# Kernel tuning notes

Measured on AMD Instinct MI355X. Metric: run time of the kernel, lower is better.

## Reference

```python
import jax, jax.numpy as jnp
import numpy as np

B, Lq, Lkv = 4, 1024, 4096
Cq, Ckv, E, NH = 512, 512, 512, 8
HD = E // NH


def setup_inputs() -> dict:
    key = jax.random.key(0)
    ks = jax.random.split(key, 8)
    s = 0.02
    return {
        "Xq": jax.random.normal(ks[0], (B, Lq, Cq), dtype=jnp.float32),
        "Xkv": jax.random.normal(ks[1], (B, Lkv, Ckv), dtype=jnp.float32),
        "mask": jax.random.randint(ks[2], (B, Lq, 1), 0, 2, dtype=jnp.int32),
        "Wq": jax.random.normal(ks[3], (Cq, E), dtype=jnp.float32) * s,
        "bq": jnp.zeros((E,), dtype=jnp.float32),
        "Wkv": jax.random.normal(ks[4], (Ckv, 2 * E), dtype=jnp.float32) * s,
        "bkv": jnp.zeros((2 * E,), dtype=jnp.float32),
        "Wp": jax.random.normal(ks[5], (E, E), dtype=jnp.float32) * s,
        "bp": jnp.zeros((E,), dtype=jnp.float32),
        "attn_pos": jax.random.normal(ks[6], (1, NH, Lq, Lkv), dtype=jnp.float32) * s,
    }


def reference(Xq, Xkv, mask, Wq, bq, Wkv, bkv, Wp, bp, attn_pos):
    scale = HD ** -0.5
    # projections
    Q = (Xq @ Wq + bq).reshape(B, Lq, NH, HD).transpose(0, 2, 1, 3) * scale  # [B,NH,Lq,HD]
    KV = (Xkv @ Wkv + bkv).reshape(B, Lkv, 2, NH, HD)
    K = KV[:, :, 0].transpose(0, 2, 1, 3)  # [B,NH,Lkv,HD]
    V = KV[:, :, 1].transpose(0, 2, 1, 3)
    # scores + learned positional bias
    attn = jnp.einsum('bhqd,bhkd->bhqk', Q, K) + attn_pos  # [B,NH,Lq,Lkv]
    # dummy-column masked softmax (mask: [B,Lq,1], 1=keep row)
    m = mask.astype(attn.dtype)[:, None]           # [B,1,Lq,1]
    attn = attn + (1.0 - m) * (-100.0)             # suppress masked query rows
    dummy = jnp.broadcast_to(jnp.where(m == 0, 100.0, -100.0), (B, NH, Lq, 1))
    attn = jax.nn.softmax(jnp.concatenate([attn, dummy], axis=-1), axis=-1)[..., :Lkv]
    # weighted sum + output projection (dropout = identity in eval)
    out = jnp.einsum('bhqk,bhkd->bhqd', attn, V)
    out = out.transpose(0, 2, 1, 3).reshape(B, Lq, E)
    return out @ Wp + bp
```

## Files before the change

### kernel.cpp

```cpp
#include <hip/hip_runtime.h>

typedef unsigned short u16;
typedef __attribute__((ext_vector_type(8))) short bf16x8;
typedef __attribute__((ext_vector_type(4))) float f32x4;
typedef __attribute__((ext_vector_type(2))) unsigned u32x2;
typedef __attribute__((ext_vector_type(4))) unsigned u32x4;

__device__ __forceinline__ u16 f2bf(float x) {
    union { float f; unsigned u; } v; v.f = x;
    unsigned r = v.u + 0x7FFF + ((v.u >> 16) & 1);
    return (u16)(r >> 16);
}

__device__ __forceinline__ unsigned cvt_pk_bf16(float lo, float hi) {
    unsigned r;
    asm("v_cvt_pk_bf16_f32 %0, %1, %2" : "=v"(r) : "v"(lo), "v"(hi));
    return r;
}

__device__ __forceinline__ bf16x8 pk8(const f32x4& s0, const f32x4& s1) {
    union { u32x4 u; bf16x8 v; } x;
    x.u[0] = cvt_pk_bf16(s0[0], s0[1]);
    x.u[1] = cvt_pk_bf16(s0[2], s0[3]);
    x.u[2] = cvt_pk_bf16(s1[0], s1[1]);
    x.u[3] = cvt_pk_bf16(s1[2], s1[3]);
    return x.v;
}

__device__ __forceinline__ void gl_lds16(const u16* g, u16* l) {
    __builtin_amdgcn_global_load_lds((const __attribute__((address_space(1))) void*)g,
                                     (__attribute__((address_space(3))) void*)l, 16, 0, 0);
}

__global__ __launch_bounds__(256) void prep_kernel(const float* __restrict__ Xq,
                                                   const float* __restrict__ Xkv,
                                                   u16* __restrict__ oq,
                                                   u16* __restrict__ okv,
                                                   const float* __restrict__ Wq,
                                                   const float* __restrict__ Wkv,
                                                   const float* __restrict__ Wp,
                                                   u16* __restrict__ WqT,
                                                   u16* __restrict__ WkvT,
                                                   u16* __restrict__ WpT) {
    __shared__ float tile[64][65];
    int bid = blockIdx.x;
    int tid = threadIdx.x;
    if (bid < 5120) {
        const float* in;
        u16* out;
        size_t i;
        if (bid < 1024) {
            in = Xq; out = oq;
            i = ((size_t)bid * 256 + tid) * 8;
        } else {
            in = Xkv; out = okv;
            i = ((size_t)(bid - 1024) * 256 + tid) * 8;
        }
        const float4* p = (const float4*)(in + i);
        float4 a = p[0], b = p[1];
        u32x4 w = {cvt_pk_bf16(a.x, a.y), cvt_pk_bf16(a.z, a.w),
                   cvt_pk_bf16(b.x, b.y), cvt_pk_bf16(b.z, b.w)};
        *(u32x4*)(out + i) = w;
        return;
    }
    bid -= 5120;
    const float* in;
    u16* out;
    int R = 512, C, bx, by;
    if (bid < 64) {
        in = Wq; out = WqT; C = 512; bx = bid & 7; by = bid >> 3;
    } else if (bid < 192) {
        bid -= 64;
        in = Wkv; out = WkvT; C = 1024; bx = bid & 15; by = bid >> 4;
    } else {
        bid -= 192;
        in = Wp; out = WpT; C = 512; bx = bid & 7; by = bid >> 3;
    }
    int r0 = by * 64, c0 = bx * 64;
#pragma unroll
    for (int j = 0; j < 16; ++j) {
        int e = tid + j * 256;
        int row = e >> 6, col = e & 63;
        tile[row][col] = in[(size_t)(r0 + row) * C + c0 + col];
    }
    __syncthreads();
#pragma unroll
    for (int j = 0; j < 16; ++j) {
        int e = tid + j * 256;
        int row = e >> 6, col = e & 63;
        out[(size_t)(c0 + row) * R + r0 + col] = f2bf(tile[col][row]);
    }
}

__global__ __launch_bounds__(256) void gemm_qkv(const u16* __restrict__ Xqb,
                                                const u16* __restrict__ WqT,
                                                const float* __restrict__ bq,
                                                u16* __restrict__ Qb,
                                                const u16* __restrict__ Xkvb,
                                                const u16* __restrict__ WkvT,
                                                const float* __restrict__ bkv,
                                                u16* __restrict__ Kb,
                                                u16* __restrict__ Vt) {
    __shared__ u16 Al[128][64];
    __shared__ u16 Bl[128][64];
    int tid = threadIdx.x;
    int lane = tid & 63, wid = tid >> 6;
    int wr = wid >> 1, wc = wid & 1;
    int l15 = lane & 15, g = lane >> 4;
    int ldr = lane >> 3, ldc = (lane & 7) << 3;
    int bid = blockIdx.x;

    if (bid < 256) {
        int bn = bid & 7, bm = bid >> 3;
        const int K = 512;
        f32x4 acc[4][2];
#pragma unroll
        for (int m = 0; m < 4; ++m)
#pragma unroll
            for (int n = 0; n < 2; ++n)
#pragma unroll
                for (int j = 0; j < 4; ++j) acc[m][n][j] = 0.f;

        for (int kt = 0; kt < 8; ++kt) {
            __syncthreads();
#pragma unroll
            for (int i = 0; i < 6; ++i) {
                int c = wid * 6 + i;
                if (c < 16) {
                    int row = c * 8 + ldr;
                    gl_lds16(Xqb + (size_t)(bm * 128 + row) * K + kt * 64 + ldc,
                             &Al[0][0] + c * 512);
                } else {
                    int cb = c - 16;
                    int row = cb * 8 + ldr;
                    gl_lds16(WqT + (size_t)(bn * 64 + row) * K + kt * 64 + ldc,
                             &Bl[0][0] + cb * 512);
                }
            }
            __syncthreads();

#pragma unroll
            for (int kk = 0; kk < 2; ++kk) {
                bf16x8 af[4], bfr[2];
#pragma unroll
                for (int m = 0; m < 4; ++m)
                    af[m] = *(const bf16x8*)&Al[wr * 64 + m * 16 + l15][kk * 32 + g * 8];
#pragma unroll
                for (int n = 0; n < 2; ++n)
                    bfr[n] = *(const bf16x8*)&Bl[wc * 32 + n * 16 + l15][kk * 32 + g * 8];
#pragma unroll
                for (int m = 0; m < 4; ++m)
#pragma unroll
                    for (int n = 0; n < 2; ++n)
                        acc[m][n] = __builtin_amdgcn_mfma_f32_16x16x32_bf16(af[m], bfr[n],
                                                                            acc[m][n], 0, 0, 0);
            }
        }

#pragma unroll
        for (int m = 0; m < 4; ++m)
#pragma unroll
            for (int n = 0; n < 2; ++n)
#pragma unroll
                for (int j = 0; j < 4; ++j) {
                    int row = bm * 128 + wr * 64 + m * 16 + g * 4 + j;
                    int col = bn * 64 + wc * 32 + n * 16 + l15;
                    float v = acc[m][n][j] + bq[col];
                    int b = row >> 10, q = row & 1023, h = col >> 6, d = col & 63;
                    Qb[(((size_t)((b * 8 + h) * 1024 + q)) << 6) + d] =
                        f2bf(v * 0.18033688011112042f);
                }
    } else {
        int b2 = bid - 256;
        int bn = b2 & 7, bm = b2 >> 3;
        const int K = 512;
        f32x4 acc[4][4];
#pragma unroll
        for (int m = 0; m < 4; ++m)
#pragma unroll
            for (int n = 0; n < 4; ++n)
#pragma unroll
                for (int j = 0; j < 4; ++j) acc[m][n][j] = 0.f;

        for (int kt = 0; kt < 8; ++kt) {
            __syncthreads();
#pragma unroll
            for (int i = 0; i < 4; ++i) {
                int c = wid * 4 + i;
                int row = c * 8 + ldr;
                gl_lds16(Xkvb + (size_t)(bm * 128 + row) * K + kt * 64 + ldc,
                         &Al[0][0] + c * 512);
                gl_lds16(WkvT + (size_t)(bn * 128 + row) * K + kt * 64 + ldc,
                         &Bl[0][0] + c * 512);
            }
            __syncthreads();

#pragma unroll
            for (int kk = 0; kk < 2; ++kk) {
                bf16x8 af[4], bfr[4];
#pragma unroll
                for (int m = 0; m < 4; ++m)
                    af[m] = *(const bf16x8*)&Al[wr * 64 + m * 16 + l15][kk * 32 + g * 8];
#pragma unroll
                for (int n = 0; n < 4; ++n)
                    bfr[n] = *(const bf16x8*)&Bl[wc * 64 + n * 16 + l15][kk * 32 + g * 8];
#pragma unroll
                for (int m = 0; m < 4; ++m)
#pragma unroll
                    for (int n = 0; n < 4; ++n)
                        acc[m][n] = __builtin_amdgcn_mfma_f32_16x16x32_bf16(af[m], bfr[n],
                                                                            acc[m][n], 0, 0, 0);
            }
        }

#pragma unroll
        for (int m = 0; m < 4; ++m)
#pragma unroll
            for (int n = 0; n < 4; ++n)
#pragma unroll
                for (int j = 0; j < 4; ++j) {
                    int row = bm * 128 + wr * 64 + m * 16 + g * 4 + j;
                    int col = bn * 128 + wc * 64 + n * 16 + l15;
                    float v = acc[m][n][j] + bkv[col];
                    int b = row >> 12, kv = row & 4095;
                    if (col < 512) {
                        int h = col >> 6, d = col & 63;
                        Kb[(((size_t)((b * 8 + h) * 4096 + kv)) << 6) + d] = f2bf(v);
                    } else {
                        int c2 = col - 512;
                        int h = c2 >> 6, d = c2 & 63;
                        int p = j | ((m & 1) << 2) | (g << 3);
                        int dkv = (kv & ~31) | p;
                        Vt[((size_t)(b * 8 + h) * 64 + d) * 4096 + dkv] = f2bf(v);
                    }
                }
    }
}

__global__ __launch_bounds__(256) void gemm_out(const u16* __restrict__ A,
                                                const u16* __restrict__ Bt,
                                                const float* __restrict__ bias,
                                                float* __restrict__ Cout,
                                                int M, int N, int K) {
    __shared__ u16 Al[128][64];
    __shared__ u16 Bl[64][64];
    int tid = threadIdx.x;
    int lane = tid & 63, wid = tid >> 6;
    int wr = wid >> 1, wc = wid & 1;
    int l15 = lane & 15, g = lane >> 4;
    int bm = blockIdx.y, bn = blockIdx.x;
    int ldr = lane >> 3, ldc = (lane & 7) << 3;

    f32x4 acc[4][2];
#pragma unroll
    for (int m = 0; m < 4; ++m)
#pragma unroll
        for (int n = 0; n < 2; ++n)
#pragma unroll
            for (int j = 0; j < 4; ++j) acc[m][n][j] = 0.f;

    int nK = K >> 6;
    for (int kt = 0; kt < nK; ++kt) {
        __syncthreads();
#pragma unroll
        for (int i = 0; i < 6; ++i) {
            int c = wid * 6 + i;
            if (c < 16) {
                int row = c * 8 + ldr;
                gl_lds16(A + (size_t)(bm * 128 + row) * K + kt * 64 + ldc, &Al[0][0] + c * 512);
            } else {
                int cb = c - 16;
                int row = cb * 8 + ldr;
                gl_lds16(Bt + (size_t)(bn * 64 + row) * K + kt * 64 + ldc, &Bl[0][0] + cb * 512);
            }
        }
        __syncthreads();

#pragma unroll
        for (int kk = 0; kk < 2; ++kk) {
            bf16x8 af[4], bfr[2];
#pragma unroll
            for (int m = 0; m < 4; ++m)
                af[m] = *(const bf16x8*)&Al[wr * 64 + m * 16 + l15][kk * 32 + g * 8];
#pragma unroll
            for (int n = 0; n < 2; ++n)
                bfr[n] = *(const bf16x8*)&Bl[wc * 32 + n * 16 + l15][kk * 32 + g * 8];
#pragma unroll
            for (int m = 0; m < 4; ++m)
#pragma unroll
                for (int n = 0; n < 2; ++n)
                    acc[m][n] =
                        __builtin_amdgcn_mfma_f32_16x16x32_bf16(af[m], bfr[n], acc[m][n], 0, 0, 0);
        }
    }

#pragma unroll
    for (int m = 0; m < 4; ++m)
#pragma unroll
        for (int n = 0; n < 2; ++n)
#pragma unroll
            for (int j = 0; j < 4; ++j) {
                int row = bm * 128 + wr * 64 + m * 16 + g * 4 + j;
                int col = bn * 64 + wc * 32 + n * 16 + l15;
                Cout[(size_t)row * N + col] = acc[m][n][j] + bias[col];
            }
}

__global__ __launch_bounds__(256, 2) void attn_kernel(const u16* __restrict__ Qb,
                                                      const u16* __restrict__ Kb,
                                                      const u16* __restrict__ Vt,
                                                      const float* __restrict__ pos,
                                                      float* __restrict__ Opart,
                                                      float* __restrict__ Lp) {
    __shared__ u16 Klds[4][4096];
    __shared__ u16 Vlds[4][4096];

    int idx = blockIdx.x;
    int h = idx & 7;
    int rest = idx >> 3;
    int qt = rest & 15, sp = rest >> 4;
    int q0 = qt * 64;
    int kvbase = sp * 1024;
    int tid = threadIdx.x, lane = tid & 63, wid = tid >> 6;
    int l15 = lane & 15, g = lane >> 4;

    bf16x8 aq[4][2];
#pragma unroll
    for (int b = 0; b < 4; ++b) {
        const u16* qp =
            Qb + (((size_t)((b * 8 + h) * 1024 + q0 + wid * 16 + l15)) << 6) + g * 8;
        aq[b][0] = *(const bf16x8*)(qp);
        aq[b][1] = *(const bf16x8*)(qp + 32);
    }

    f32x4 o[4][4];
    f32x4 lacc[4];
#pragma unroll
    for (int b = 0; b < 4; ++b) {
#pragma unroll
        for (int j = 0; j < 4; ++j) lacc[b][j] = 0.f;
#pragma unroll
        for (int n = 0; n < 4; ++n)
#pragma unroll
            for (int j = 0; j < 4; ++j) o[b][n][j] = 0.f;
    }

    const u16* Kg = Kb + ((size_t)(wid * 8 + h)) * 4096 * 64;
    const u16* Vg = Vt + ((size_t)(wid * 8 + h)) * 4096 * 64;
    u16* KldsW = &Klds[wid][0];
    u16* VldsW = &Vlds[wid][0];
    int lr = lane >> 3;
    int lcs = ((lane & 7) ^ lr) << 3;

    const float* posq =
        pos + (size_t)h * 1024 * 4096 + (size_t)(q0 + wid * 16 + l15) * 4096 + kvbase;

    const short one_s = (short)0x3F80;
    bf16x8 ones = {one_s, one_s, one_s, one_s, one_s, one_s, one_s, one_s};
    int sw = (l15 & 7) << 4;

    f32x4 zr[4];
    for (int kt = 0; kt < 16; ++kt) {
        int kv0 = kvbase + kt * 64;
        __syncthreads();
#pragma unroll
        for (int c = 0; c < 8; ++c)
            gl_lds16(Kg + (size_t)(kv0 + c * 8 + lr) * 64 + lcs, KldsW + c * 512);
#pragma unroll
        for (int c = 0; c < 8; ++c)
            gl_lds16(Vg + (size_t)(c * 8 + lr) * 4096 + kv0 + lcs, VldsW + c * 512);
#pragma unroll
        for (int n = 0; n < 4; ++n) {
            zr[n] = *(const f32x4*)(posq + kt * 64 + n * 16 + g * 4);
#pragma unroll
            for (int j = 0; j < 4; ++j) zr[n][j] *= 1.44269504f;
        }
        __syncthreads();

#pragma unroll
        for (int b = 0; b < 4; ++b) {
            const char* KbL = (const char*)&Klds[b][0];
            const char* VbL = (const char*)&Vlds[b][0];

            f32x4 s[4];
            __builtin_amdgcn_s_setprio(1);
#pragma unroll
            for (int n = 0; n < 4; ++n) {
                bf16x8 kb0 = *(const bf16x8*)(KbL + (n * 16 + l15) * 128 + ((g * 16) ^ sw));
                bf16x8 kb1 = *(const bf16x8*)(KbL + (n * 16 + l15) * 128 + ((64 + g * 16) ^ sw));
                f32x4 t = __builtin_amdgcn_mfma_f32_16x16x32_bf16(kb0, aq[b][0], zr[n], 0, 0, 0);
                s[n] = __builtin_amdgcn_mfma_f32_16x16x32_bf16(kb1, aq[b][1], t, 0, 0, 0);
            }
            __builtin_amdgcn_s_setprio(0);

#pragma unroll
            for (int n = 0; n < 4; ++n)
#pragma unroll
                for (int j = 0; j < 4; ++j) s[n][j] = __builtin_exp2f(s[n][j]);

            bf16x8 pa0 = pk8(s[0], s[1]);
            bf16x8 pa1 = pk8(s[2], s[3]);

            __builtin_amdgcn_s_setprio(1);
#pragma unroll
            for (int n = 0; n < 4; ++n) {
                bf16x8 vb0 = *(const bf16x8*)(VbL + (n * 16 + l15) * 128 + ((g * 16) ^ sw));
                bf16x8 vb1 = *(const bf16x8*)(VbL + (n * 16 + l15) * 128 + ((64 + g * 16) ^ sw));
                o[b][n] = __builtin_amdgcn_mfma_f32_16x16x32_bf16(pa0, vb0, o[b][n], 0, 0, 0);
                o[b][n] = __builtin_amdgcn_mfma_f32_16x16x32_bf16(pa1, vb1, o[b][n], 0, 0, 0);
            }
            lacc[b] = __builtin_amdgcn_mfma_f32_16x16x32_bf16(pa0, ones, lacc[b], 0, 0, 0);
            lacc[b] = __builtin_amdgcn_mfma_f32_16x16x32_bf16(pa1, ones, lacc[b], 0, 0, 0);
            __builtin_amdgcn_s_setprio(0);
        }
    }

#pragma unroll
    for (int b = 0; b < 4; ++b) {
        int obase = (sp * 32 + b * 8 + h) * 1024;
#pragma unroll
        for (int j = 0; j < 4; ++j) {
            int row = q0 + wid * 16 + g * 4 + j;
#pragma unroll
            for (int n = 0; n < 4; ++n)
                __builtin_nontemporal_store(o[b][n][j],
                                            &Opart[((size_t)(obase + row)) * 64 + n * 16 + l15]);
            if (l15 == 0) __builtin_nontemporal_store(lacc[b][j], &Lp[obase + row]);
        }
    }
}

__global__ __launch_bounds__(256) void attn_combine(const float* __restrict__ Opart,
                                                    const float* __restrict__ Lp,
                                                    const int* __restrict__ mask,
                                                    u16* __restrict__ AO) {
    int tid = threadIdx.x;
    int d0 = (tid & 15) << 2;
    int r = blockIdx.x * 16 + (tid >> 4);
    int bh = r >> 10, q = r & 1023;
    int b = bh >> 3, h = bh & 7;

    float L = 0.f;
    f32x4 val = {0.f, 0.f, 0.f, 0.f};
#pragma unroll
    for (int s2 = 0; s2 < 4; ++s2) {
        size_t rr = (size_t)(s2 * 32 + bh) * 1024 + q;
        L += Lp[rr];
        f32x4 v = *(const f32x4*)(Opart + rr * 64 + d0);
#pragma unroll
        for (int j = 0; j < 4; ++j) val[j] += v[j];
    }
    float inv = mask[b * 1024 + q] ? (1.0f / L) : 0.f;
    u32x2 w;
    w.x = cvt_pk_bf16(val[0] * inv, val[1] * inv);
    w.y = cvt_pk_bf16(val[2] * inv, val[3] * inv);
    *(u32x2*)(AO + ((size_t)(b * 1024 + q)) * 512 + h * 64 + d0) = w;
}

extern "C" void kernel_launch(void* const* d_in, const int* in_sizes, int n_in,
                              void* d_out, int out_size, void* d_ws, size_t ws_size,
                              hipStream_t stream) {
    const float* Xq = (const float*)d_in[0];
    const float* Xkv = (const float*)d_in[1];
    const int* mask = (const int*)d_in[2];
    const float* Wq = (const float*)d_in[3];
    const float* bq = (const float*)d_in[4];
    const float* Wkv = (const float*)d_in[5];
    const float* bkv = (const float*)d_in[6];
    const float* Wp = (const float*)d_in[7];
    const float* bp = (const float*)d_in[8];
    const float* pos = (const float*)d_in[9];
    float* out = (float*)d_out;

    char* ws = (char*)d_ws;
    u16* WqT = (u16*)(ws);
    u16* WkvT = (u16*)(ws + 524288);
    u16* WpT = (u16*)(ws + 1572864);
    u16* Qb = (u16*)(ws + 2097152);
    u16* Kb = (u16*)(ws + 6291456);
    u16* Vt = (u16*)(ws + 23068672);
    u16* AO = (u16*)(ws + 39845888);
    float* Opart = (float*)(ws + 44040192);
    u16* Xkvb = (u16*)(ws + 44040192);
    u16* Xqb = (u16*)(ws + 60817408);
    float* Lp = (float*)(ws + 111149056);

    prep_kernel<<<dim3(5376), 256, 0, stream>>>(Xq, Xkv, Xqb, Xkvb, Wq, Wkv, Wp, WqT, WkvT,
                                                WpT);
    gemm_qkv<<<dim3(1280), 256, 0, stream>>>(Xqb, WqT, bq, Qb, Xkvb, WkvT, bkv, Kb, Vt);
    attn_kernel<<<dim3(512), 256, 0, stream>>>(Qb, Kb, Vt, pos, Opart, Lp);
    attn_combine<<<dim3(2048), 256, 0, stream>>>(Opart, Lp, mask, AO);
    gemm_out<<<dim3(8, 32), 256, 0, stream>>>(AO, WpT, bp, out, 4096, 512, 512);
}
```

Baseline: 172.4 us.

## Double-buffer K/V LDS tiles with 32-wide KV steps in attention kernel

Splits each KV tile into 32-key halves held in two LDS buffers, so global-to-LDS loads for the next step are issued before computing the current one, using explicit vmcnt waits and raw barriers. The V tile gets a new interleaved, swizzled layout so each 16-row MFMA reads a single bf16x8 fragment. The aim is to hide global load latency that the old load-then-sync loop left exposed. In exchange there are twice as many barriers and loop iterations, and correctness depends on a hand-tuned waitcnt.

Measured after the change: 179.3 us. +4.0%, slower.

```diff
diff --git a/kernel.cpp b/kernel.cpp
--- a/kernel.cpp
+++ b/kernel.cpp
@@ -312,8 +312,8 @@
                                                       const float* __restrict__ pos,
                                                       float* __restrict__ Opart,
                                                       float* __restrict__ Lp) {
-    __shared__ u16 Klds[4][4096];
-    __shared__ u16 Vlds[4][4096];
+    __shared__ u16 Klds[2][4][2048];
+    __shared__ u16 Vlds[2][4][2048];
 
     int idx = blockIdx.x;
     int h = idx & 7;
@@ -347,10 +347,10 @@
 
     const u16* Kg = Kb + ((size_t)(wid * 8 + h)) * 4096 * 64;
     const u16* Vg = Vt + ((size_t)(wid * 8 + h)) * 4096 * 64;
-    u16* KldsW = &Klds[wid][0];
-    u16* VldsW = &Vlds[wid][0];
     int lr = lane >> 3;
     int lcs = ((lane & 7) ^ lr) << 3;
+    int vhalf = (lane >> 2) & 1;
+    int vslot = (lane & 3) ^ (lr & 3);
 
     const float* posq =
         pos + (size_t)h * 1024 * 4096 + (size_t)(q0 + wid * 16 + l15) * 4096 + kvbase;
@@ -359,33 +359,52 @@
     bf16x8 ones = {one_s, one_s, one_s, one_s, one_s, one_s, one_s, one_s};
     int sw = (l15 & 7) << 4;
 
-    f32x4 zr[4];
-    for (int kt = 0; kt < 16; ++kt) {
-        int kv0 = kvbase + kt * 64;
-        __syncthreads();
-#pragma unroll
-        for (int c = 0; c < 8; ++c)
-            gl_lds16(Kg + (size_t)(kv0 + c * 8 + lr) * 64 + lcs, KldsW + c * 512);
-#pragma unroll
-        for (int c = 0; c < 8; ++c)
-            gl_lds16(Vg + (size_t)(c * 8 + lr) * 4096 + kv0 + lcs, VldsW + c * 512);
-#pragma unroll
-        for (int n = 0; n < 4; ++n) {
-            zr[n] = *(const f32x4*)(posq + kt * 64 + n * 16 + g * 4);
+    auto STAGE = [&](int buf, int t) {
+        int kv0 = kvbase + t * 32;
+#pragma unroll
+        for (int c = 0; c < 4; ++c) {
+            gl_lds16(Kg + (size_t)(kv0 + c * 8 + lr) * 64 + lcs, &Klds[buf][wid][c * 512]);
+            gl_lds16(Vg + (size_t)(2 * (c * 8 + lr) + vhalf) * 4096 + kv0 + vslot * 8,
+                     &Vlds[buf][wid][c * 512]);
+        }
+    };
+
+    STAGE(0, 0);
+
+    for (int kt = 0; kt < 32; ++kt) {
+        int cur = kt & 1;
+        __builtin_amdgcn_s_barrier();
+        f32x4 zr[2];
+#pragma unroll
+        for (int n = 0; n < 2; ++n)
+            zr[n] = *(const f32x4*)(posq + kt * 32 + n * 16 + g * 4);
+        __builtin_amdgcn_sched_barrier(0);
+        if (kt < 31) {
+            STAGE(cur ^ 1, kt + 1);
+            __builtin_amdgcn_sched_barrier(0);
+            asm volatile("s_waitcnt vmcnt(8)" ::: "memory");
+        } else {
+            __builtin_amdgcn_sched_barrier(0);
+            asm volatile("s_waitcnt vmcnt(0)" ::: "memory");
+        }
+        __builtin_amdgcn_sched_barrier(0);
+        __builtin_amdgcn_s_barrier();
+        __builtin_amdgcn_sched_barrier(0);
+
+#pragma unroll
+        for (int n = 0; n < 2; ++n)
 #pragma unroll
             for (int j = 0; j < 4; ++j) zr[n][j] *= 1.44269504f;
-        }
-        __syncthreads();
 
 #pragma unroll
         for (int b = 0; b < 4; ++b) {
-            const char* KbL = (const char*)&Klds[b][0];
-            const char* VbL = (const char*)&Vlds[b][0];
-
-            f32x4 s[4];
+            const char* KbL = (const char*)&Klds[cur][b][0];
+            const char* VbL = (const char*)&Vlds[cur][b][0];
+
+            f32x4 s[2];
             __builtin_amdgcn_s_setprio(1);
 #pragma unroll
-            for (int n = 0; n < 4; ++n) {
+            for (int n = 0; n < 2; ++n) {
                 bf16x8 kb0 = *(const bf16x8*)(KbL + (n * 16 + l15) * 128 + ((g * 16) ^ sw));
                 bf16x8 kb1 = *(const bf16x8*)(KbL + (n * 16 + l15) * 128 + ((64 + g * 16) ^ sw));
                 f32x4 t = __builtin_amdgcn_mfma_f32_16x16x32_bf16(kb0, aq[b][0], zr[n], 0, 0, 0);
@@ -394,23 +413,22 @@
             __builtin_amdgcn_s_setprio(0);
 
 #pragma unroll
-            for (int n = 0; n < 4; ++n)
+            for (int n = 0; n < 2; ++n)
 #pragma unroll
                 for (int j = 0; j < 4; ++j) s[n][j] = __builtin_exp2f(s[n][j]);
 
-            bf16x8 pa0 = pk8(s[0], s[1]);
-            bf16x8 pa1 = pk8(s[2], s[3]);
+            bf16x8 pa = pk8(s[0], s[1]);
 
             __builtin_amdgcn_s_setprio(1);
 #pragma unroll
             for (int n = 0; n < 4; ++n) {
-                bf16x8 vb0 = *(const bf16x8*)(VbL + (n * 16 + l15) * 128 + ((g * 16) ^ sw));
-                bf16x8 vb1 = *(const bf16x8*)(VbL + (n * 16 + l15) * 128 + ((64 + g * 16) ^ sw));
-                o[b][n] = __builtin_amdgcn_mfma_f32_16x16x32_bf16(pa0, vb0, o[b][n], 0, 0, 0);
-                o[b][n] = __builtin_amdgcn_mfma_f32_16x16x32_bf16(pa1, vb1, o[b][n], 0, 0, 0);
-            }
-            lacc[b] = __builtin_amdgcn_mfma_f32_16x16x32_bf16(pa0, ones, lacc[b], 0, 0, 0);
-            lacc[b] = __builtin_amdgcn_mfma_f32_16x16x32_bf16(pa1, ones, lacc[b], 0, 0, 0);
+                int vd = n * 16 + l15;
+                int vr = vd >> 1;
+                int vbyte = (vr << 7) + ((vd & 1) << 6) + (((g ^ (vr & 3)) & 3) << 4);
+                bf16x8 vb = *(const bf16x8*)(VbL + vbyte);
+                o[b][n] = __builtin_amdgcn_mfma_f32_16x16x32_bf16(pa, vb, o[b][n], 0, 0, 0);
+            }
+            lacc[b] = __builtin_amdgcn_mfma_f32_16x16x32_bf16(pa, ones, lacc[b], 0, 0, 0);
             __builtin_amdgcn_s_setprio(0);
         }
     }
```
